# Performance work log

Measured on AMD Instinct MI355X. Metric: run time of the kernel, lower is better.

The kernel has to match this reference:

```python
import jax, jax.numpy as jnp
import numpy as np

B, T = 32, 256
CHAR_V, BICHAR_V, CTYPE_V = 10000, 200000, 8
CD, BD, TD = 100, 100, 20
LIN, H = 200, 200
IN_DIMS = 2 * CD + 2 * BD + TD  # 420


def lstm_scan(xs, Wih, Whh, b, reverse=False):
    # xs: [T, B, LIN]; Wih: [4H, LIN]; Whh: [4H, H]; b: [4H]
    h0 = jnp.zeros((xs.shape[1], Whh.shape[1]), xs.dtype)
    c0 = jnp.zeros_like(h0)

    def step(carry, x):
        h, c = carry
        g = x @ Wih.T + h @ Whh.T + b  # [B, 4H]
        i, f, gg, o = jnp.split(g, 4, axis=-1)  # torch LSTMCell gate order
        c = jax.nn.sigmoid(f) * c + jax.nn.sigmoid(i) * jnp.tanh(gg)
        h = jax.nn.sigmoid(o) * jnp.tanh(c)
        return (h, c), h

    _, hs = jax.lax.scan(step, (h0, c0), xs, reverse=reverse)
    return hs  # [T, B, H]


def setup_inputs() -> dict:
    key = jax.random.key(0)
    ks = jax.random.split(key, 20)
    d = {
        "chars": jax.random.randint(ks[0], (B, T), 0, CHAR_V, jnp.int32),
        "left_bichar": jax.random.randint(ks[1], (B, T), 0, BICHAR_V, jnp.int32),
        "right_bichar": jax.random.randint(ks[2], (B, T), 0, BICHAR_V, jnp.int32),
        "extchars": jax.random.randint(ks[3], (B, T), 0, CHAR_V, jnp.int32),
        "extleft_bichar": jax.random.randint(ks[4], (B, T), 0, BICHAR_V, jnp.int32),
        "extright_bichar": jax.random.randint(ks[5], (B, T), 0, BICHAR_V, jnp.int32),
        "char_type": jax.random.randint(ks[6], (B, T), 0, CTYPE_V, jnp.int32),
        "E_char": jax.random.normal(ks[7], (CHAR_V, CD), jnp.float32) * 0.1,
        "E_extchar": jax.random.normal(ks[8], (CHAR_V, CD), jnp.float32) * 0.1,
        "E_bichar": jax.random.normal(ks[9], (BICHAR_V, BD), jnp.float32) * 0.1,
        "E_extbichar": jax.random.normal(ks[10], (BICHAR_V, BD), jnp.float32) * 0.1,
        "E_ctype": jax.random.normal(ks[11], (CTYPE_V, TD), jnp.float32) * 0.1,
        "fc_w": jax.random.normal(ks[12], (LIN, IN_DIMS), jnp.float32) * (1.0 / np.sqrt(IN_DIMS)),
        "fc_b": jnp.zeros((LIN,), jnp.float32),
        "Wih_l": jax.random.normal(ks[13], (4 * H, LIN), jnp.float32) * (1.0 / np.sqrt(LIN)),
        "Whh_l": jax.random.normal(ks[14], (4 * H, H), jnp.float32) * (1.0 / np.sqrt(H)),
        "b_l": jnp.zeros((4 * H,), jnp.float32),
        "Wih_r": jax.random.normal(ks[15], (4 * H, LIN), jnp.float32) * (1.0 / np.sqrt(LIN)),
        "Whh_r": jax.random.normal(ks[16], (4 * H, H), jnp.float32) * (1.0 / np.sqrt(H)),
        "b_r": jnp.zeros((4 * H,), jnp.float32),
    }
    return d


def reference(chars, left_bichar, right_bichar, extchars, extleft_bichar,
              extright_bichar, char_type, E_char, E_extchar, E_bichar,
              E_extbichar, E_ctype, fc_w, fc_b, Wih_l, Whh_l, b_l,
              Wih_r, Whh_r, b_r):
    c_e = E_char[chars]            # [B,T,CD]
    ec_e = E_extchar[extchars]
    lb_e = E_bichar[left_bichar]   # [B,T,BD]
    elb_e = E_extbichar[extleft_bichar]
    rb_e = E_bichar[right_bichar]
    erb_e = E_extbichar[extright_bichar]
    ct_e = E_ctype[char_type]      # [B,T,TD]

    left_total = jnp.concatenate([c_e, ec_e, lb_e, elb_e, ct_e], axis=2)
    right_total = jnp.concatenate([c_e, ec_e, rb_e, erb_e, ct_e], axis=2)

    left_x = jnp.tanh(left_total @ fc_w.T + fc_b).transpose(1, 0, 2)   # [T,B,LIN]
    right_x = jnp.tanh(right_total @ fc_w.T + fc_b).transpose(1, 0, 2)

    left_hs = lstm_scan(left_x, Wih_l, Whh_l, b_l, reverse=False)   # [T,B,H]
    right_hs = lstm_scan(right_x, Wih_r, Whh_r, b_r, reverse=True)  # [T,B,H]

    out = jnp.concatenate([left_hs, right_hs], axis=2).transpose(1, 0, 2)  # [B,T,2H]
    return out
```

## Files before the change

### kernel.cpp

```cpp
#include <hip/hip_runtime.h>
#include <stdint.h>

#define B_    32
#define T_    256
#define CD    100
#define BD    100
#define TD    20
#define LIN   200
#define HD    200
#define INDIM 420
#define G4    800

typedef __attribute__((ext_vector_type(8))) short bfrag8;
typedef __attribute__((ext_vector_type(4))) float f32x4v;

static __device__ __forceinline__ unsigned short f2bf(float f) {
  unsigned u = __float_as_uint(f);
  u = u + 0x7fffu + ((u >> 16) & 1u);
  return (unsigned short)(u >> 16);
}
static __device__ __forceinline__ float bf2f(unsigned short s) {
  return __uint_as_float(((unsigned)s) << 16);
}
static __device__ __forceinline__ float tanhx(float x) {
  return 1.0f - 2.0f * __builtin_amdgcn_rcpf(1.0f + __builtin_amdgcn_exp2f(x * 2.8853900817779268f));
}
static __device__ __forceinline__ float clamp40(float x) {
  return fminf(fmaxf(x, -40.0f), 40.0f);
}

static __device__ __forceinline__ void mk_hilo(float4 a, float4 b, bfrag8& hi, bfrag8& lo) {
  float q[8] = {a.x, a.y, a.z, a.w, b.x, b.y, b.z, b.w};
  #pragma unroll
  for (int j = 0; j < 8; ++j) {
    unsigned short h = f2bf(q[j]);
    hi[j] = (short)h;
    lo[j] = (short)f2bf(q[j] - bf2f(h));
  }
}
static __device__ __forceinline__ bfrag8 mk_hi(float4 a, float4 b) {
  bfrag8 r;
  float q[8] = {a.x, a.y, a.z, a.w, b.x, b.y, b.z, b.w};
  #pragma unroll
  for (int j = 0; j < 8; ++j) r[j] = (short)f2bf(q[j]);
  return r;
}

__global__ void presplit_kernel(const float* __restrict__ fc_w,
                                const float* __restrict__ Wih_l,
                                const float* __restrict__ Wih_r,
                                unsigned short* __restrict__ fcw_hi,
                                unsigned short* __restrict__ fcw_lo,
                                unsigned short* __restrict__ wih_hi,
                                unsigned short* __restrict__ wih_lo) {
  int tid = blockIdx.x * blockDim.x + threadIdx.x;
  int stride = gridDim.x * blockDim.x;
  for (int i = tid; i < 13 * 14 * 512; i += stride) {
    int j = i & 7, l = (i >> 3) & 63, f = i >> 9;
    int kt = f % 14, nt = f / 14;
    int n = nt * 16 + (l & 15);
    int k = kt * 32 + ((l >> 4) << 3) + j;
    float v = (n < LIN && k < INDIM) ? fc_w[n * INDIM + k] : 0.0f;
    unsigned short h = f2bf(v);
    fcw_hi[i] = h;
    fcw_lo[i] = f2bf(v - bf2f(h));
  }
  for (int d = 0; d < 2; ++d) {
    const float* W = d ? Wih_r : Wih_l;
    unsigned short* oh = wih_hi + (size_t)d * 179200;
    unsigned short* ol = wih_lo + (size_t)d * 179200;
    for (int i = tid; i < 50 * 7 * 512; i += stride) {
      int j = i & 7, l = (i >> 3) & 63, f = i >> 9;
      int kt = f % 7, nt = f / 7;
      int np = nt * 16 + (l & 15);
      int no = (np & 3) * 200 + (np >> 2);
      int k = kt * 32 + ((l >> 4) << 3) + j;
      float v = (k < LIN) ? W[no * LIN + k] : 0.0f;
      unsigned short h = f2bf(v);
      oh[i] = h;
      ol[i] = f2bf(v - bf2f(h));
    }
  }
}

__global__ __launch_bounds__(256) void fc_kernel(
    const int* __restrict__ chars, const int* __restrict__ left_bichar,
    const int* __restrict__ right_bichar, const int* __restrict__ extchars,
    const int* __restrict__ extleft, const int* __restrict__ extright,
    const int* __restrict__ ctype,
    const float* __restrict__ E_char, const float* __restrict__ E_extchar,
    const float* __restrict__ E_bichar, const float* __restrict__ E_extbichar,
    const float* __restrict__ E_ctype, const float* __restrict__ fc_b,
    const unsigned short* __restrict__ fcw_hi, const unsigned short* __restrict__ fcw_lo,
    float* __restrict__ x) {
  __shared__ __align__(16) float feat[32 * 452];
  int rb = blockIdx.x;
  int dir = rb >> 8;
  int t = rb & 255;
  int tid = threadIdx.x;
  const int* bi  = dir ? right_bichar : left_bichar;
  const int* ebi = dir ? extright : extleft;

  for (int cc = tid; cc < 32 * 113; cc += 256) {
    int lr = cc / 113, kc = cc - lr * 113;
    int k = kc << 2;
    float4 v = make_float4(0.f, 0.f, 0.f, 0.f);
    if (k < INDIM) {
      int id; const float* tab; int kk; int wdt;
      if (k < 100)      { id = chars[lr * T_ + t];    tab = E_char;      kk = k;       wdt = 100; }
      else if (k < 200) { id = extchars[lr * T_ + t]; tab = E_extchar;   kk = k - 100; wdt = 100; }
      else if (k < 300) { id = bi[lr * T_ + t];       tab = E_bichar;    kk = k - 200; wdt = 100; }
      else if (k < 400) { id = ebi[lr * T_ + t];      tab = E_extbichar; kk = k - 300; wdt = 100; }
      else              { id = ctype[lr * T_ + t];    tab = E_ctype;     kk = k - 400; wdt = 20;  }
      v = *reinterpret_cast<const float4*>(tab + (size_t)id * wdt + kk);
    }
    *reinterpret_cast<float4*>(&feat[lr * 452 + k]) = v;
  }
  __syncthreads();

  int w = tid >> 6, l = tid & 63;
  int lrow = l & 15, lk8 = (l >> 4) << 3;
  f32x4v acc[8];
  #pragma unroll
  for (int i = 0; i < 8; ++i) acc[i] = (f32x4v){0.f, 0.f, 0.f, 0.f};

  for (int kt = 0; kt < 14; ++kt) {
    bfrag8 ah[2], al[2];
    #pragma unroll
    for (int mt = 0; mt < 2; ++mt) {
      const float* fp = &feat[(mt * 16 + lrow) * 452 + kt * 32 + lk8];
      float4 v0 = *reinterpret_cast<const float4*>(fp);
      float4 v1 = *reinterpret_cast<const float4*>(fp + 4);
      mk_hilo(v0, v1, ah[mt], al[mt]);
    }
    #pragma unroll
    for (int s = 0; s < 4; ++s) {
      int nt = w + (s << 2);
      if (nt < 13) {
        size_t fo = ((size_t)(nt * 14 + kt) * 64 + l) * 8;
        bfrag8 bh = *reinterpret_cast<const bfrag8*>(fcw_hi + fo);
        bfrag8 bl = *reinterpret_cast<const bfrag8*>(fcw_lo + fo);
        #pragma unroll
        for (int mt = 0; mt < 2; ++mt) {
          acc[s * 2 + mt] = __builtin_amdgcn_mfma_f32_16x16x32_bf16(ah[mt], bh, acc[s * 2 + mt], 0, 0, 0);
          acc[s * 2 + mt] = __builtin_amdgcn_mfma_f32_16x16x32_bf16(al[mt], bh, acc[s * 2 + mt], 0, 0, 0);
          acc[s * 2 + mt] = __builtin_amdgcn_mfma_f32_16x16x32_bf16(ah[mt], bl, acc[s * 2 + mt], 0, 0, 0);
        }
      }
    }
  }
  int r0 = rb * 32;
  #pragma unroll
  for (int s = 0; s < 4; ++s) {
    int nt = w + (s << 2);
    if (nt < 13) {
      int n = nt * 16 + lrow;
      if (n < LIN) {
        float bias = fc_b[n];
        #pragma unroll
        for (int mt = 0; mt < 2; ++mt) {
          #pragma unroll
          for (int rr = 0; rr < 4; ++rr) {
            int row = mt * 16 + ((l >> 4) << 2) + rr;
            x[(size_t)(r0 + row) * LIN + n] = tanhx(acc[s * 2 + mt][rr] + bias);
          }
        }
      }
    }
  }
}

__global__ __launch_bounds__(512) void xwih_kernel(
    const float* __restrict__ x, const unsigned short* __restrict__ wih_hi,
    const unsigned short* __restrict__ wih_lo, const float* __restrict__ b_l,
    const float* __restrict__ b_r, float* __restrict__ pre) {
  int bid = blockIdx.x;
  int dir = (bid >= 320) ? 1 : 0;
  int rem = bid - dir * 320;
  int rbm = rem / 5, nb = rem - rbm * 5;
  int m0 = rbm * 128, n0 = nb * 160;
  int tid = threadIdx.x, w = tid >> 6, l = tid & 63;
  int lrow = l & 15, lk8 = (l >> 4) << 3;
  const float* xd = x + (size_t)dir * 8192 * LIN;
  const unsigned short* wh = wih_hi + (size_t)dir * 179200;
  const unsigned short* wl = wih_lo + (size_t)dir * 179200;
  const float* bias = dir ? b_r : b_l;

  f32x4v acc[10];
  #pragma unroll
  for (int i = 0; i < 10; ++i) acc[i] = (f32x4v){0.f, 0.f, 0.f, 0.f};

  int row = m0 + w * 16 + lrow;
  for (int kt = 0; kt < 7; ++kt) {
    int kb = kt * 32 + lk8;
    bfrag8 ah = {0,0,0,0,0,0,0,0}, al = {0,0,0,0,0,0,0,0};
    if (kb <= 192) {
      const float* fp = xd + (size_t)row * LIN + kb;
      float4 v0 = *reinterpret_cast<const float4*>(fp);
      float4 v1 = *reinterpret_cast<const float4*>(fp + 4);
      mk_hilo(v0, v1, ah, al);
    }
    #pragma unroll
    for (int nt = 0; nt < 10; ++nt) {
      int ntg = nb * 10 + nt;
      size_t fo = ((size_t)(ntg * 7 + kt) * 64 + l) * 8;
      bfrag8 bh = *reinterpret_cast<const bfrag8*>(wh + fo);
      bfrag8 bl = *reinterpret_cast<const bfrag8*>(wl + fo);
      acc[nt] = __builtin_amdgcn_mfma_f32_16x16x32_bf16(ah, bh, acc[nt], 0, 0, 0);
      acc[nt] = __builtin_amdgcn_mfma_f32_16x16x32_bf16(al, bh, acc[nt], 0, 0, 0);
      acc[nt] = __builtin_amdgcn_mfma_f32_16x16x32_bf16(ah, bl, acc[nt], 0, 0, 0);
    }
  }
  #pragma unroll
  for (int nt = 0; nt < 10; ++nt) {
    int n = n0 + nt * 16 + lrow;
    float bb = bias[(n & 3) * 200 + (n >> 2)];
    int hcol = n >> 2, g = n & 3;
    int tau = hcol >> 2;
    int lhi = hcol & 3;
    #pragma unroll
    for (int rr = 0; rr < 4; ++rr) {
      int r2 = m0 + w * 16 + ((l >> 4) << 2) + rr;
      int t = r2 >> 5, b32 = r2 & 31;
      int hf2 = b32 >> 4, b = b32 & 15;
      int lane = b + 16 * lhi;
      size_t dst = ((((size_t)(dir * 2 + hf2) * 256 + t) * 50 + tau) * 64 + lane) * 4 + g;
      pre[dst] = acc[nt][rr] + bb;
    }
  }
}

__global__ __launch_bounds__(512, 2) void lstm_kernel(
    const float* __restrict__ pre, const float* __restrict__ Whh_l,
    const float* __restrict__ Whh_r, float* __restrict__ out) {
  __shared__ __align__(16) unsigned short hbufA[3584];
  __shared__ __align__(16) unsigned short hbufB[3584];
  __shared__ __align__(16) unsigned short whx[7168];
  __shared__ __align__(16) float pbuf0[12800];
  __shared__ __align__(16) float pbuf1[12800];

  int bi = blockIdx.x;
  int dir = bi >> 1, half = bi & 1;
  const float* Whh = dir ? Whh_r : Whh_l;
  int tid = threadIdx.x, w = tid >> 6, l = tid & 63;
  int lrow = l & 15, lk8 = (l >> 4) << 3;

  bfrag8 Breg[6][7];
  #pragma unroll
  for (int i = 0; i < 6; ++i) {
    int np = (w + 8 * i) * 16 + lrow;
    int no = (np & 3) * 200 + (np >> 2);
    #pragma unroll
    for (int kt = 0; kt < 7; ++kt) {
      int kb = kt * 32 + lk8;
      bfrag8 bb = {0,0,0,0,0,0,0,0};
      if (kb <= 192) {
        const float* fp = Whh + (size_t)no * HD + kb;
        bb = mk_hi(*reinterpret_cast<const float4*>(fp),
                   *reinterpret_cast<const float4*>(fp + 4));
      }
      Breg[i][kt] = bb;
    }
  }
  for (int e = tid; e < 896; e += 512) {
    int l2 = e & 63, f = e >> 6;
    int kt = f % 7, tile = f / 7;
    int np = (48 + tile) * 16 + (l2 & 15);
    int no = (np & 3) * 200 + (np >> 2);
    int kb = kt * 32 + ((l2 >> 4) << 3);
    bfrag8 bb = {0,0,0,0,0,0,0,0};
    if (kb <= 192) {
      const float* fp = Whh + (size_t)no * HD + kb;
      bb = mk_hi(*reinterpret_cast<const float4*>(fp),
                 *reinterpret_cast<const float4*>(fp + 4));
    }
    *reinterpret_cast<bfrag8*>(&whx[(size_t)e * 8]) = bb;
  }
  for (int e = tid; e < 896; e += 512) {
    reinterpret_cast<uint64_t*>(hbufA)[e] = 0;
    reinterpret_cast<uint64_t*>(hbufB)[e] = 0;
  }
  float c[7];
  #pragma unroll
  for (int i = 0; i < 7; ++i) c[i] = 0.f;

  int hbase = 4 * w + (l >> 4);
  int hw = (lrow + 16 * ((hbase >> 3) & 3)) * 8 + (hbase & 7);

  const char* psrcB = (const char*)(pre
                      + ((size_t)(dir * 2 + half) * 256 + (dir ? 255 : 0)) * 12800)
                    + l * 16;
  const int pstepB = dir ? -51200 : 51200;
  float* outp = out + (size_t)((half * 16 + lrow) * 256 + (dir ? 255 : 0)) * 400
              + dir * 200 + (l >> 4) + 4 * w;
  const int ostep = dir ? -400 : 400;

  __syncthreads();

  #pragma unroll
  for (int i = 0; i < 6; ++i)
    __builtin_amdgcn_global_load_lds(
        (const __attribute__((address_space(1))) void*)(psrcB + (8 * i + w) * 1024),
        (__attribute__((address_space(3))) void*)(&pbuf0[(8 * i + w) * 256]), 16, 0, 0);
  if (w < 2)
    __builtin_amdgcn_global_load_lds(
        (const __attribute__((address_space(1))) void*)(psrcB + (48 + w) * 1024),
        (__attribute__((address_space(3))) void*)(&pbuf0[(48 + w) * 256]), 16, 0, 0);
  psrcB += pstepB;
  asm volatile("s_waitcnt vmcnt(0)");
  __syncthreads();

  const float NL  = -1.4426950408889634f;
  const float N2L = -2.8853900817779268f;

  auto STEP = [&](const unsigned short* rbuf, unsigned short* wbuf,
                  const float* pcur, float* pnxt) {
    #pragma unroll
    for (int i = 0; i < 6; ++i)
      __builtin_amdgcn_global_load_lds(
          (const __attribute__((address_space(1))) void*)(psrcB + (8 * i + w) * 1024),
          (__attribute__((address_space(3))) void*)(pnxt + (8 * i + w) * 256), 16, 0, 0);
    if (w < 2)
      __builtin_amdgcn_global_load_lds(
          (const __attribute__((address_space(1))) void*)(psrcB + (48 + w) * 1024),
          (__attribute__((address_space(3))) void*)(pnxt + (48 + w) * 256), 16, 0, 0);
    psrcB += pstepB;
    __builtin_amdgcn_sched_barrier(0x1 | 0x2 | 0x4 | 0x8);
    if (w < 2) { asm volatile("s_waitcnt vmcnt(14)"); }
    else       { asm volatile("s_waitcnt vmcnt(12)"); }
    __builtin_amdgcn_sched_barrier(0x1 | 0x2 | 0x4 | 0x8);
    bfrag8 hf[7];
    #pragma unroll
    for (int kt = 0; kt < 7; ++kt)
      hf[kt] = *reinterpret_cast<const bfrag8*>(&rbuf[kt * 512 + l * 8]);
    __builtin_amdgcn_s_setprio(1);
    #pragma unroll
    for (int i = 0; i < 7; ++i) {
      if (i < 6 || w < 2) {
        int tau = (i < 6) ? (8 * i + w) : (48 + w);
        f32x4v a = *reinterpret_cast<const f32x4v*>(pcur + tau * 256 + l * 4);
        #pragma unroll
        for (int kt = 0; kt < 7; ++kt) {
          bfrag8 bb;
          if (i < 6) bb = Breg[i][kt];
          else       bb = *reinterpret_cast<const bfrag8*>(&whx[(w * 7 + kt) * 512 + l * 8]);
          a = __builtin_amdgcn_mfma_f32_16x16x32_bf16(bb, hf[kt], a, 0, 0, 0);
        }
        float u  = __builtin_amdgcn_exp2f(clamp40(a[1] * NL));
        float v  = __builtin_amdgcn_exp2f(clamp40(a[0] * NL));
        float Wt = __builtin_amdgcn_exp2f(clamp40(a[2] * N2L));
        float y  = __builtin_amdgcn_exp2f(clamp40(a[3] * NL));
        float pu = 1.f + u, pv = 1.f + v, pw = 1.f + Wt, py = 1.f + y;
        float P  = pv * pw;
        float r1 = __builtin_amdgcn_rcpf(pu * P);
        float cn = (c[i] * P + pu * (1.f - Wt)) * r1;
        c[i] = cn;
        float Z  = __builtin_amdgcn_exp2f(clamp40(cn * N2L));
        float h  = (1.f - Z) * __builtin_amdgcn_rcpf(py * (1.f + Z));
        outp[32 * i] = h;
        wbuf[hw + i * 512] = f2bf(h);
      }
    }
    __builtin_amdgcn_s_setprio(0);
    outp += ostep;
    __builtin_amdgcn_sched_barrier(0x1 | 0x2 | 0x4 | 0x8);
    asm volatile("s_waitcnt lgkmcnt(0)");
    __builtin_amdgcn_s_barrier();
    __builtin_amdgcn_sched_barrier(0x1 | 0x2 | 0x4 | 0x8);
  };

  for (int it = 0; it < 128; ++it) {
    STEP(hbufA, hbufB, pbuf0, pbuf1);
    STEP(hbufB, hbufA, pbuf1, pbuf0);
  }
}

extern "C" void kernel_launch(void* const* d_in, const int* in_sizes, int n_in,
                              void* d_out, int out_size, void* d_ws, size_t ws_size,
                              hipStream_t stream) {
  (void)in_sizes; (void)n_in; (void)out_size; (void)ws_size;
  const int* chars        = (const int*)d_in[0];
  const int* left_bichar  = (const int*)d_in[1];
  const int* right_bichar = (const int*)d_in[2];
  const int* extchars     = (const int*)d_in[3];
  const int* extleft      = (const int*)d_in[4];
  const int* extright     = (const int*)d_in[5];
  const int* ctype        = (const int*)d_in[6];
  const float* E_char      = (const float*)d_in[7];
  const float* E_extchar   = (const float*)d_in[8];
  const float* E_bichar    = (const float*)d_in[9];
  const float* E_extbichar = (const float*)d_in[10];
  const float* E_ctype     = (const float*)d_in[11];
  const float* fc_w  = (const float*)d_in[12];
  const float* fc_b  = (const float*)d_in[13];
  const float* Wih_l = (const float*)d_in[14];
  const float* Whh_l = (const float*)d_in[15];
  const float* b_l   = (const float*)d_in[16];
  const float* Wih_r = (const float*)d_in[17];
  const float* Whh_r = (const float*)d_in[18];
  const float* b_r   = (const float*)d_in[19];
  float* out = (float*)d_out;
  char* ws = (char*)d_ws;

  float* x   = (float*)(ws);
  float* pre = (float*)(ws + 13107200);
  unsigned short* fcw_hi = (unsigned short*)(ws + 65536000);
  unsigned short* fcw_lo = (unsigned short*)(ws + 65722368);
  unsigned short* wih_hi = (unsigned short*)(ws + 65908736);
  unsigned short* wih_lo = (unsigned short*)(ws + 66625536);

  presplit_kernel<<<256, 256, 0, stream>>>(fc_w, Wih_l, Wih_r, fcw_hi, fcw_lo, wih_hi, wih_lo);
  fc_kernel<<<512, 256, 0, stream>>>(chars, left_bichar, right_bichar, extchars,
                                     extleft, extright, ctype, E_char, E_extchar,
                                     E_bichar, E_extbichar, E_ctype, fc_b,
                                     fcw_hi, fcw_lo, x);
  xwih_kernel<<<640, 512, 0, stream>>>(x, wih_hi, wih_lo, b_l, b_r, pre);
  lstm_kernel<<<4, 512, 0, stream>>>(pre, Whh_l, Whh_r, out);
}
```

Baseline: 663.9 us.

## Fold gate log2 scales into weights and prefetch preactivations into registers

The sigmoid/tanh exp2 scale factors are folded into the input-projection output and the bf16 recurrent weights, so the per-step multiplies disappear. The LDS double-buffered global_load_lds prefetch of preactivations is replaced by a one-step register prefetch, which frees about 100KB of shared memory. The bf16 conversion of h uses the hardware v_cvt_pk_bf16_f32 instruction. This risks exposed global-load latency inside the serial recurrence and adds register pressure, and scaling before bf16 rounding changes precision slightly.

```diff
diff --git a/kernel.cpp b/kernel.cpp
--- a/kernel.cpp
+++ b/kernel.cpp
@@ -11,6 +11,9 @@
 #define INDIM 420
 #define G4    800
 
+#define NLs  (-1.4426950408889634f)
+#define N2Ls (-2.8853900817779268f)
+
 typedef __attribute__((ext_vector_type(8))) short bfrag8;
 typedef __attribute__((ext_vector_type(4))) float f32x4v;
 
@@ -28,6 +31,9 @@
 static __device__ __forceinline__ float clamp40(float x) {
   return fminf(fmaxf(x, -40.0f), 40.0f);
 }
+static __device__ __forceinline__ float exp2c(float x) {
+  return __builtin_amdgcn_exp2f(clamp40(x));
+}
 
 static __device__ __forceinline__ void mk_hilo(float4 a, float4 b, bfrag8& hi, bfrag8& lo) {
   float q[8] = {a.x, a.y, a.z, a.w, b.x, b.y, b.z, b.w};
@@ -44,6 +50,9 @@
   #pragma unroll
   for (int j = 0; j < 8; ++j) r[j] = (short)f2bf(q[j]);
   return r;
+}
+static __device__ __forceinline__ float4 scale4(float4 v, float s) {
+  return make_float4(v.x * s, v.y * s, v.z * s, v.w * s);
 }
 
 __global__ void presplit_kernel(const float* __restrict__ fc_w,
@@ -216,6 +225,7 @@
     int n = n0 + nt * 16 + lrow;
     float bb = bias[(n & 3) * 200 + (n >> 2)];
     int hcol = n >> 2, g = n & 3;
+    float sg = (g == 2) ? N2Ls : NLs;
     int tau = hcol >> 2;
     int lhi = hcol & 3;
     #pragma unroll
@@ -225,7 +235,7 @@
       int hf2 = b32 >> 4, b = b32 & 15;
       int lane = b + 16 * lhi;
       size_t dst = ((((size_t)(dir * 2 + hf2) * 256 + t) * 50 + tau) * 64 + lane) * 4 + g;
-      pre[dst] = acc[nt][rr] + bb;
+      pre[dst] = (acc[nt][rr] + bb) * sg;
     }
   }
 }
@@ -236,8 +246,6 @@
   __shared__ __align__(16) unsigned short hbufA[3584];
   __shared__ __align__(16) unsigned short hbufB[3584];
   __shared__ __align__(16) unsigned short whx[7168];
-  __shared__ __align__(16) float pbuf0[12800];
-  __shared__ __align__(16) float pbuf1[12800];
 
   int bi = blockIdx.x;
   int dir = bi >> 1, half = bi & 1;
@@ -250,14 +258,15 @@
   for (int i = 0; i < 6; ++i) {
     int np = (w + 8 * i) * 16 + lrow;
     int no = (np & 3) * 200 + (np >> 2);
+    float sg = ((np & 3) == 2) ? N2Ls : NLs;
     #pragma unroll
     for (int kt = 0; kt < 7; ++kt) {
       int kb = kt * 32 + lk8;
       bfrag8 bb = {0,0,0,0,0,0,0,0};
       if (kb <= 192) {
         const float* fp = Whh + (size_t)no * HD + kb;
-        bb = mk_hi(*reinterpret_cast<const float4*>(fp),
-                   *reinterpret_cast<const float4*>(fp + 4));
+        bb = mk_hi(scale4(*reinterpret_cast<const float4*>(fp), sg),
+                   scale4(*reinterpret_cast<const float4*>(fp + 4), sg));
       }
       Breg[i][kt] = bb;
     }
@@ -267,12 +276,13 @@
     int kt = f % 7, tile = f / 7;
     int np = (48 + tile) * 16 + (l2 & 15);
     int no = (np & 3) * 200 + (np >> 2);
+    float sg = ((np & 3) == 2) ? N2Ls : NLs;
     int kb = kt * 32 + ((l2 >> 4) << 3);
     bfrag8 bb = {0,0,0,0,0,0,0,0};
     if (kb <= 192) {
       const float* fp = Whh + (size_t)no * HD + kb;
-      bb = mk_hi(*reinterpret_cast<const float4*>(fp),
-                 *reinterpret_cast<const float4*>(fp + 4));
+      bb = mk_hi(scale4(*reinterpret_cast<const float4*>(fp), sg),
+                 scale4(*reinterpret_cast<const float4*>(fp + 4), sg));
     }
     *reinterpret_cast<bfrag8*>(&whx[(size_t)e * 8]) = bb;
   }
@@ -287,48 +297,28 @@
   int hbase = 4 * w + (l >> 4);
   int hw = (lrow + 16 * ((hbase >> 3) & 3)) * 8 + (hbase & 7);
 
-  const char* psrcB = (const char*)(pre
-                      + ((size_t)(dir * 2 + half) * 256 + (dir ? 255 : 0)) * 12800)
-                    + l * 16;
-  const int pstepB = dir ? -51200 : 51200;
+  const float* ps = pre + ((size_t)(dir * 2 + half) * 256 + (dir ? 255 : 0)) * 12800
+                  + l * 4;
+  const int pstep = dir ? -12800 : 12800;
   float* outp = out + (size_t)((half * 16 + lrow) * 256 + (dir ? 255 : 0)) * 400
               + dir * 200 + (l >> 4) + 4 * w;
   const int ostep = dir ? -400 : 400;
 
   __syncthreads();
 
-  #pragma unroll
-  for (int i = 0; i < 6; ++i)
-    __builtin_amdgcn_global_load_lds(
-        (const __attribute__((address_space(1))) void*)(psrcB + (8 * i + w) * 1024),
-        (__attribute__((address_space(3))) void*)(&pbuf0[(8 * i + w) * 256]), 16, 0, 0);
-  if (w < 2)
-    __builtin_amdgcn_global_load_lds(
-        (const __attribute__((address_space(1))) void*)(psrcB + (48 + w) * 1024),
-        (__attribute__((address_space(3))) void*)(&pbuf0[(48 + w) * 256]), 16, 0, 0);
-  psrcB += pstepB;
-  asm volatile("s_waitcnt vmcnt(0)");
-  __syncthreads();
-
-  const float NL  = -1.4426950408889634f;
-  const float N2L = -2.8853900817779268f;
-
-  auto STEP = [&](const unsigned short* rbuf, unsigned short* wbuf,
-                  const float* pcur, float* pnxt) {
-    #pragma unroll
-    for (int i = 0; i < 6; ++i)
-      __builtin_amdgcn_global_load_lds(
-          (const __attribute__((address_space(1))) void*)(psrcB + (8 * i + w) * 1024),
-          (__attribute__((address_space(3))) void*)(pnxt + (8 * i + w) * 256), 16, 0, 0);
-    if (w < 2)
-      __builtin_amdgcn_global_load_lds(
-          (const __attribute__((address_space(1))) void*)(psrcB + (48 + w) * 1024),
-          (__attribute__((address_space(3))) void*)(pnxt + (48 + w) * 256), 16, 0, 0);
-    psrcB += pstepB;
-    __builtin_amdgcn_sched_barrier(0x1 | 0x2 | 0x4 | 0x8);
-    if (w < 2) { asm volatile("s_waitcnt vmcnt(14)"); }
-    else       { asm volatile("s_waitcnt vmcnt(12)"); }
-    __builtin_amdgcn_sched_barrier(0x1 | 0x2 | 0x4 | 0x8);
+  f32x4v pc[7];
+  #pragma unroll
+  for (int i = 0; i < 7; ++i) {
+    if (i < 6 || w < 2) {
+      int tau = (i < 6) ? (8 * i + w) : (48 + w);
+      pc[i] = *reinterpret_cast<const f32x4v*>(ps + tau * 256);
+    } else {
+      pc[i] = (f32x4v){0.f, 0.f, 0.f, 0.f};
+    }
+  }
+  ps += pstep;
+
+  auto STEP = [&](const unsigned short* rbuf, unsigned short* wbuf) {
     bfrag8 hf[7];
     #pragma unroll
     for (int kt = 0; kt < 7; ++kt)
@@ -338,7 +328,8 @@
     for (int i = 0; i < 7; ++i) {
       if (i < 6 || w < 2) {
         int tau = (i < 6) ? (8 * i + w) : (48 + w);
-        f32x4v a = *reinterpret_cast<const f32x4v*>(pcur + tau * 256 + l * 4);
+        f32x4v a = pc[i];
+        pc[i] = *reinterpret_cast<const f32x4v*>(ps + tau * 256);
         #pragma unroll
         for (int kt = 0; kt < 7; ++kt) {
           bfrag8 bb;
@@ -346,22 +337,25 @@
           else       bb = *reinterpret_cast<const bfrag8*>(&whx[(w * 7 + kt) * 512 + l * 8]);
           a = __builtin_amdgcn_mfma_f32_16x16x32_bf16(bb, hf[kt], a, 0, 0, 0);
         }
-        float u  = __builtin_amdgcn_exp2f(clamp40(a[1] * NL));
-        float v  = __builtin_amdgcn_exp2f(clamp40(a[0] * NL));
-        float Wt = __builtin_amdgcn_exp2f(clamp40(a[2] * N2L));
-        float y  = __builtin_amdgcn_exp2f(clamp40(a[3] * NL));
+        float u  = exp2c(a[1]);
+        float v  = exp2c(a[0]);
+        float Wt = exp2c(a[2]);
+        float y  = exp2c(a[3]);
         float pu = 1.f + u, pv = 1.f + v, pw = 1.f + Wt, py = 1.f + y;
         float P  = pv * pw;
         float r1 = __builtin_amdgcn_rcpf(pu * P);
         float cn = (c[i] * P + pu * (1.f - Wt)) * r1;
         c[i] = cn;
-        float Z  = __builtin_amdgcn_exp2f(clamp40(cn * N2L));
+        float Z  = exp2c(cn * N2Ls);
         float h  = (1.f - Z) * __builtin_amdgcn_rcpf(py * (1.f + Z));
         outp[32 * i] = h;
-        wbuf[hw + i * 512] = f2bf(h);
+        unsigned hb;
+        asm("v_cvt_pk_bf16_f32 %0, %1, %2" : "=v"(hb) : "v"(h), "v"(h));
+        wbuf[hw + i * 512] = (unsigned short)hb;
       }
     }
     __builtin_amdgcn_s_setprio(0);
+    ps += pstep;
     outp += ostep;
     __builtin_amdgcn_sched_barrier(0x1 | 0x2 | 0x4 | 0x8);
     asm volatile("s_waitcnt lgkmcnt(0)");
@@ -370,8 +364,8 @@
   };
 
   for (int it = 0; it < 128; ++it) {
-    STEP(hbufA, hbufB, pbuf0, pbuf1);
-    STEP(hbufB, hbufA, pbuf1, pbuf0);
+    STEP(hbufA, hbufB);
+    STEP(hbufB, hbufA);
   }
 }
 
```

Result: slower. 727.2 us (+9.5%).
